# Kernel tuning notes

Measured on AMD Instinct MI355X. Metric: run time of the kernel, lower is better.

## Reference

```python
import jax, jax.numpy as jnp
import numpy as np

BATCH, MAXPV = 32, 50
RULENUM, PROPNUM = 256, 256  # must be equal (eye(rulenum) * property_importance)
ENT_DIM, RULE_DIM = 128, 128
ENTITYNUM = 50000
THRESHOLD = 0.5


def _l2norm(x, eps=1e-12):
    # F.normalize(p=2, dim=-1)
    n = jnp.linalg.norm(x, axis=-1, keepdims=True)
    return x / jnp.clip(n, eps)


def setup_inputs() -> dict:
    key = jax.random.key(0)
    ks = jax.random.split(key, 20)
    d_in = ENT_DIM + RULE_DIM
    inp = {
        'property': jax.random.randint(ks[0], (BATCH, MAXPV), 0, ENTITYNUM),
        'value': jax.random.randint(ks[1], (BATCH, MAXPV), 0, ENTITYNUM),
        'samemask': jax.random.randint(ks[2], (BATCH, MAXPV), 0, 2),
        'padmask': jax.random.randint(ks[3], (BATCH, MAXPV), 0, 2),
        'rule_embedding': jax.random.normal(ks[4], (RULENUM, RULE_DIM), jnp.float32),
        'entity_table': jax.random.normal(ks[5], (ENTITYNUM, ENT_DIM), jnp.float32),
        # Linear weights stored (in, out); concat order in the original is (p_emb, rule_emb)
        'fc1_w': jax.random.normal(ks[6], (d_in, ENT_DIM), jnp.float32),
        'fc1_b': jax.random.normal(ks[7], (ENT_DIM,), jnp.float32) * 0.02,
        'fc2_w': jax.random.normal(ks[8], (d_in, ENT_DIM), jnp.float32),
        'fc2_b': jax.random.normal(ks[9], (ENT_DIM,), jnp.float32) * 0.02,
        'fc3_w': jax.random.normal(ks[10], (d_in, ENT_DIM), jnp.float32),
        'fc3_b': jax.random.normal(ks[11], (ENT_DIM,), jnp.float32) * 0.02,
        'fc4_w': jax.random.normal(ks[12], (ENT_DIM, 1), jnp.float32) * 0.05,
        'fc4_b': jax.random.normal(ks[13], (1,), jnp.float32) * 0.02,
        'fc5_w': jax.random.normal(ks[14], (ENT_DIM, 1), jnp.float32) * 0.05,
        'fc5_b': jax.random.normal(ks[15], (1,), jnp.float32) * 0.02,
        'fc6_w': jax.random.normal(ks[16], (ENT_DIM, ENT_DIM), jnp.float32) * 0.05,
        'fc6_b': jax.random.normal(ks[17], (ENT_DIM,), jnp.float32) * 0.02,
    }
    return inp


def reference(property, value, samemask, padmask, rule_embedding, entity_table,
              fc1_w, fc1_b, fc2_w, fc2_b, fc3_w, fc3_b,
              fc4_w, fc4_b, fc5_w, fc5_b, fc6_w, fc6_b):
    E = entity_table.shape[1]
    R = rule_embedding.shape[0]
    P = R  # propertynum == rulenum (required by eye() regularizer)

    p_emb = _l2norm(entity_table[property])   # (B, M, E)
    v_emb = _l2norm(entity_table[value])      # (B, M, E)
    r_emb = _l2norm(rule_embedding)           # (R, Dr)

    # cat(p, rule) -> Linear decomposed into two smaller matmuls (same math)
    def branch(w, b):
        return p_emb @ w[:E], r_emb @ w[E:] + b  # (B,M,Eo), (R,Eo)

    # s1 branch
    pa, ra = branch(fc1_w, fc1_b)
    h1 = jax.nn.relu(pa[:, None, :, :] + ra[None, :, None, :])   # (B,R,M,E)
    s1 = jax.nn.sigmoid(h1 @ fc4_w + fc4_b)[..., 0]              # (B,R,M)

    # p branch
    pb, rb = branch(fc2_w, fc2_b)
    h2 = jax.nn.relu(pb[:, None, :, :] + rb[None, :, None, :])
    p = jax.nn.sigmoid(h2 @ fc5_w + fc5_b)[..., 0]               # (B,R,M)

    # s2 branch
    pc, rc = branch(fc3_w, fc3_b)
    h3 = jax.nn.relu(pc[:, None, :, :] + rc[None, :, None, :])
    gv = _l2norm(h3 @ fc6_w + fc6_b)                             # (B,R,M,E)
    vb = v_emb[:, None, :, :]                                    # (B,1,M,E)
    denom = jnp.clip(jnp.linalg.norm(vb, axis=-1) * jnp.linalg.norm(gv, axis=-1), 1e-8)
    cos = jnp.sum(vb * gv, axis=-1) / denom
    s2 = 0.5 * cos + 0.5                                         # (B,R,M)

    score = p + (1.0 - p) * s2
    score = jnp.where(samemask[:, None, :] == 1, s1 * score, 1.0 - s1)

    # property importance K: fc1/fc4 on cat(prop_emb, rule_emb)
    prop_emb = _l2norm(entity_table[:P])                         # propertyids = arange(P)
    pi_h = jax.nn.relu((prop_emb @ fc1_w[:E])[None, :, :]
                       + (r_emb @ fc1_w[E:] + fc1_b)[:, None, :])  # (R,P,E)
    pi = jax.nn.sigmoid(pi_h @ fc4_w + fc4_b)[..., 0]            # (R,P)

    rule_mask = jnp.sum(pi * (pi > THRESHOLD), axis=-1) + 1.0    # (R,)

    score = score * padmask[:, None, :].astype(score.dtype)
    score = score * (s1 > THRESHOLD)
    score = jnp.sum(score, axis=-1) / rule_mask[None, :]          # (B,R)
    pooledscore = jnp.max(score, axis=1)                          # (B,)

    diag = jnp.eye(R, dtype=pi.dtype)
    reg = pi * diag + (1.0 - pi) * (1.0 - diag)
    reg = -jnp.log(reg + 1e-8) * (1.0 - diag + diag * R)
    reg_logits = jnp.mean(reg)
    return pooledscore, reg_logits
```

## Files before the change

kernel.cpp:

```cpp
#include <hip/hip_runtime.h>
#include <hip/hip_bf16.h>

#define BATCH 32
#define MAXPV 50
#define RN 256
#define PN 256
#define DIM 128
#define NI (BATCH*MAXPV)

typedef unsigned short u16;
typedef __attribute__((ext_vector_type(8))) short short8;
typedef __attribute__((ext_vector_type(4))) float f32x4;

__device__ float g_pa[NI*DIM], g_pb[NI*DIM], g_pc[NI*DIM];
__device__ float g_pp1[PN*DIM];
__device__ __attribute__((aligned(16))) float g_v[NI*DIM];
__device__ __attribute__((aligned(16))) float g_ra[RN*DIM];
__device__ __attribute__((aligned(16))) float g_rb[RN*DIM];
__device__ float g_rmask[RN], g_regp[RN];
__device__ float g_scores[(size_t)NI*RN];
__device__ short8 g_bfrag[8][4][64];
__device__ __attribute__((aligned(16))) float g_rcA[16*4*64*8];

#define WS_WLS(ws)  ((ws)+4)
#define WS_WLD(ws)  ((ws)+4+1600)

__device__ __forceinline__ float bf2f(u16 u){ return __uint_as_float(((unsigned)u)<<16); }
__device__ __forceinline__ float LD(const void* p, size_t i, bool bf){
    return bf ? bf2f(((const u16*)p)[i]) : ((const float*)p)[i];
}
__device__ __forceinline__ int LDI(const void* p, size_t i, bool w64){
    return w64 ? (int)((const long long*)p)[i] : ((const int*)p)[i];
}
__device__ __forceinline__ short f2bf(float f){
    unsigned u = __float_as_uint(f);
    u = (u + 0x7FFFu + ((u>>16)&1u)) >> 16;
    return (short)u;
}
__device__ __forceinline__ unsigned f2bf2(float x, float y){
    float2 f; f.x=x; f.y=y;
    __hip_bfloat162 h = __float22bfloat162_rn(f);
    union { __hip_bfloat162 h; unsigned u; } c; c.h=h; return c.u;
}
__device__ __forceinline__ bool det_bf16(const void* ent){
    int l = threadIdx.x & 63;
    u16 v = ((const u16*)ent)[(size_t)2*(l*4)*977];
    int e = (v>>7)&0xFF;
    return __popcll(__ballot(e>=120 && e<=133)) >= 48;
}
__device__ __forceinline__ bool det_i64(const void* prop){
    int l = threadIdx.x & 63;
    bool z = (l<32) ? (((const unsigned*)prop)[2*l+1]==0u) : false;
    return __popcll(__ballot(z)) >= 30;
}
__device__ __forceinline__ float wred(float v){
#pragma unroll
    for(int o=32;o;o>>=1) v += __shfl_xor(v,o,64);
    return v;
}
__device__ __forceinline__ double wredd(double v){
#pragma unroll
    for(int o=32;o;o>>=1) v += __shfl_xor(v,o,64);
    return v;
}
__device__ __forceinline__ float wmax(float v){
#pragma unroll
    for(int o=32;o;o>>=1) v = fmaxf(v,__shfl_xor(v,o,64));
    return v;
}

__global__ __launch_bounds__(256) void k_pre(
    const void* __restrict__ ent, const void* __restrict__ rule,
    const void* __restrict__ prop, const void* __restrict__ val,
    const void* __restrict__ same, const void* __restrict__ pad,
    const void* __restrict__ fc6w,
    const void* __restrict__ fc1w, const void* __restrict__ fc2w, const void* __restrict__ fc3w,
    const void* __restrict__ fc1b, const void* __restrict__ fc2b, const void* __restrict__ fc3b,
    int* __restrict__ ws){
    const bool bf = det_bf16(ent);
    const int blk = blockIdx.x, tid = threadIdx.x;
    if(blk >= 379){
        const bool w64 = det_i64(prop);
        const int row = (blk-379)*4 + (tid>>6);
        const int l = tid & 63;
        size_t off = (size_t)LDI(val,row,w64)*DIM;
        float a = LD(ent,off+l,bf), b = LD(ent,off+l+64,bf);
        float n = fmaxf(sqrtf((float)wredd((double)a*a+(double)b*b)), 1e-12f);
        g_v[(size_t)row*DIM+l]=a/n; g_v[(size_t)row*DIM+l+64]=b/n;
        return;
    }
    if(blk >= 372){
        const bool w64 = det_i64(prop);
        int i = (blk-372)*256 + tid;
        if(i < NI){
            int pd = LDI(pad,i,w64);
            if(pd==1){
                int sm = LDI(same,i,w64);
                if(sm==1){
                    int x = atomicAdd(ws+0,1);
                    WS_WLS(ws)[x] = i;
                } else {
                    int x = atomicAdd(ws+1,1);
                    WS_WLD(ws)[x] = i;
                }
            }
        }
        return;
    }
    if(blk >= 364){
        int nt = blk-364;
        int ks = tid>>6, lane = tid&63;
        int n = nt*16 + (lane&15);
        int k0 = ks*32 + (lane>>4)*8;
        short8 v;
#pragma unroll
        for(int j=0;j<8;j++) v[j] = f2bf(LD(fc6w,(size_t)(k0+j)*DIM + n, bf));
        g_bfrag[nt][ks][lane] = v;
        if(nt==0){
            g_rmask[tid] = 1.f; g_regp[tid] = 0.f;
            const bool w64 = det_i64(prop);
            if(tid==0) ws[2] = (bf?1:0) | (w64?2:0);
        }
        return;
    }
    __shared__ float s_w[64*DIM];
    __shared__ __attribute__((aligned(16))) float s_in[16*DIM];
    __shared__ float s_bias[DIM];
    const void* w; size_t woff=0; const void* bptr=nullptr;
    float* out=nullptr; int row0; int mode=0; int srcsel;
    if(blk < 300){
        int wsel = blk/100; row0 = (blk%100)*16; srcsel = 0;
        w   = (wsel==0)?fc1w:(wsel==1)?fc2w:fc3w;
        out = (wsel==0)?g_pa:(wsel==1)?g_pb:g_pc;
    } else if(blk < 348){
        int rblk = blk-300; int wsel = rblk>>4; row0 = (rblk&15)*16; srcsel = 1;
        w    = (wsel==0)?fc1w:(wsel==1)?fc2w:fc3w;
        bptr = (wsel==0)?fc1b:(wsel==1)?fc2b:fc3b;
        woff = DIM*DIM; mode = wsel+1;
    } else { row0=(blk-348)*16; w=fc1w; out=g_pp1; srcsel=2; }
    const bool w64 = (srcsel==0) ? det_i64(prop) : false;
    {
        const int l = tid & 63;
        for(int it=0; it<4; it++){
            int lr = it*4 + (tid>>6);
            int row = row0 + lr;
            const void* src; size_t off;
            if(srcsel==0){ src=ent;  off=(size_t)LDI(prop,row,w64)*DIM; }
            else if(srcsel==1){ src=rule; off=(size_t)row*DIM; }
            else { src=ent; off=(size_t)row*DIM; }
            float a = LD(src,off+l,bf), b = LD(src,off+l+64,bf);
            float n = fmaxf(sqrtf((float)wredd((double)a*a+(double)b*b)), 1e-12f);
            s_in[lr*DIM+l]=a/n; s_in[lr*DIM+l+64]=b/n;
        }
    }
    if(tid<DIM) s_bias[tid] = bptr ? LD(bptr,tid,bf) : 0.f;
    const int j = tid & 127;
    const int rb8 = (tid>>7)*8;
    double acc[8] = {0,0,0,0,0,0,0,0};
    for(int half=0; half<2; half++){
        __syncthreads();
        for(int t=tid; t<64*DIM; t+=256)
            s_w[t] = LD(w, woff + (size_t)(half*64 + (t>>7))*DIM + (t&127), bf);
        __syncthreads();
        for(int k=0;k<64;k+=4){
            const float w0 = s_w[(k+0)*DIM + j];
            const float w1 = s_w[(k+1)*DIM + j];
            const float w2 = s_w[(k+2)*DIM + j];
            const float w3 = s_w[(k+3)*DIM + j];
#pragma unroll
            for(int rr=0;rr<8;rr++){
                const float4 in4 = *(const float4*)&s_in[(rb8+rr)*DIM + half*64 + k];
                acc[rr] += (double)in4.x*(double)w0;
                acc[rr] += (double)in4.y*(double)w1;
                acc[rr] += (double)in4.z*(double)w2;
                acc[rr] += (double)in4.w*(double)w3;
            }
        }
    }
    const double bj = (double)s_bias[j];
#pragma unroll
    for(int rr=0;rr<8;rr++){
        const int row = row0 + rb8 + rr;
        const float vv = (float)(bj + acc[rr]);
        if(mode==0)      out[(size_t)row*DIM + j] = vv;
        else if(mode==1) g_ra[(size_t)row*DIM + j] = vv;
        else if(mode==2) g_rb[(size_t)row*DIM + j] = vv;
        else {
            int mt=row>>4, am=row&15, ks=j>>5, quad=(j>>3)&3, jj=j&7;
            g_rcA[((mt*4+ks)*64 + quad*16+am)*8 + jj] = vv;
        }
    }
}

__global__ __launch_bounds__(256) void k_score(
    const void* __restrict__ fc4w, const void* __restrict__ fc4b,
    const void* __restrict__ fc5w, const void* __restrict__ fc5b,
    const void* __restrict__ fc6b, const int* __restrict__ ws){
    const int blk = blockIdx.x, tid = threadIdx.x;
    const int fl = ws[2];
    const bool bf = fl & 1;
    if(blk < 64){
        __shared__ float s_a[4][DIM];
        __shared__ double s_pf4[DIM];
        const int i0 = blk*4;
        if(tid<DIM) s_pf4[tid]=(double)LD(fc4w,tid,bf);
        for(int t=tid; t<4*DIM; t+=256){
            int ii=t>>7, k=t&127;
            s_a[ii][k] = g_pp1[(size_t)(i0+ii)*DIM+k];
        }
        __syncthreads();
        const int r = tid;
        const float4* rap = (const float4*)&g_ra[(size_t)r*DIM];
        double d0=0.0, d1=0.0, d2=0.0, d3=0.0;
#pragma unroll 4
        for(int x=0; x<32; x++){
            const float4 ra = rap[x];
#pragma unroll
            for(int cc=0; cc<4; cc++){
                const int k = x*4 + cc;
                const float rav = (cc==0)?ra.x:(cc==1)?ra.y:(cc==2)?ra.z:ra.w;
                const double f4k = s_pf4[k];
                d0 += (double)fmaxf(s_a[0][k]+rav,0.f)*f4k;
                d1 += (double)fmaxf(s_a[1][k]+rav,0.f)*f4k;
                d2 += (double)fmaxf(s_a[2][k]+rav,0.f)*f4k;
                d3 += (double)fmaxf(s_a[3][k]+rav,0.f)*f4k;
            }
        }
        const double b4 = (double)LD(fc4b,0,bf);
        double d[4] = {d0,d1,d2,d3};
        float mask_sum = 0.f, reg_sum = 0.f;
#pragma unroll
        for(int ii=0;ii<4;ii++){
            int p = i0 + ii;
            double sd = d[ii] + b4;
            float piv = 1.f/(1.f+expf(-(float)sd));
            if(sd > 0.0) mask_sum += piv;
            float eff = (p==r) ? piv : (1.f - piv);
            float wgt = (p==r) ? (float)RN : 1.f;
            reg_sum += -logf(eff + 1e-8f)*wgt;
        }
        atomicAdd(&g_rmask[r], mask_sum);
        atomicAdd(&g_regp[r], reg_sum);
        return;
    }
    int w2 = blk - 64;
    const int ns4 = ws[0]*4;

    __shared__ float s_pa[DIM], s_pb[DIM], s_pc[DIM], s_v[DIM], s_f4[DIM], s_f5[DIM];
    __shared__ double s_gd[2][64];
    __shared__ float s_gq[2][64];
    __shared__ double s_pd[2][128];
    __shared__ float s_s1[64], s_p[64];
    __shared__ float s_st[64][4][2];

    if(w2 >= ns4){
        int t2 = w2 - ns4;
        if(t2 >= 2*ws[1]) return;
        const int i = WS_WLD(ws)[t2>>1];
        const int sub = t2 & 1;
        if(tid < 128){
            s_pa[tid] = g_pa[(size_t)i*DIM + tid];
            s_f4[tid] = LD(fc4w,tid,bf);
        }
        __syncthreads();
        const int rr = tid & 127, half = tid >> 7;
        const int r = sub*128 + rr;
        const float4* rap = (const float4*)&g_ra[(size_t)r*DIM + half*64];
        double d = 0.0;
#pragma unroll 4
        for(int x=0; x<16; x++){
            const float4 ra = rap[x];
            const int k = half*64 + x*4;
            d += (double)fmaxf(s_pa[k+0]+ra.x,0.f)*(double)s_f4[k+0];
            d += (double)fmaxf(s_pa[k+1]+ra.y,0.f)*(double)s_f4[k+1];
            d += (double)fmaxf(s_pa[k+2]+ra.z,0.f)*(double)s_f4[k+2];
            d += (double)fmaxf(s_pa[k+3]+ra.w,0.f)*(double)s_f4[k+3];
        }
        s_pd[half][rr] = d;
        __syncthreads();
        if(tid < 128){
            const double b4 = (double)LD(fc4b,0,bf);
            double sd = (s_pd[0][tid] + s_pd[1][tid]) + b4;
            float s1v = 1.f/(1.f+expf(-(float)sd));
            g_scores[(size_t)i*RN + sub*128 + tid] = (sd > 0.0) ? (1.f - s1v) : 0.f;
        }
        return;
    }

    const int i = WS_WLS(ws)[w2>>2];
    const int q4 = w2 & 3;

    if(tid < DIM){
        s_pa[tid] = g_pa[(size_t)i*DIM + tid];
        s_pb[tid] = g_pb[(size_t)i*DIM + tid];
        s_pc[tid] = g_pc[(size_t)i*DIM + tid];
        s_f4[tid] = LD(fc4w,tid,bf);
        s_f5[tid] = LD(fc5w,tid,bf);
    } else if(tid < 192){
        const int ll = tid - 128;
        s_v[ll]    = g_v[(size_t)i*DIM + ll];
        s_v[ll+64] = g_v[(size_t)i*DIM + ll + 64];
    }
    __syncthreads();

    const int rr = tid & 63, wv = tid >> 6;
    const int r = q4*64 + rr;
    if(wv < 2){
        const float4* rap = (const float4*)&g_ra[(size_t)r*DIM + wv*64];
        double d = 0.0;
#pragma unroll 4
        for(int x=0; x<16; x++){
            const float4 ra = rap[x];
            const int k = wv*64 + x*4;
            d += (double)fmaxf(s_pa[k+0]+ra.x,0.f)*(double)s_f4[k+0];
            d += (double)fmaxf(s_pa[k+1]+ra.y,0.f)*(double)s_f4[k+1];
            d += (double)fmaxf(s_pa[k+2]+ra.z,0.f)*(double)s_f4[k+2];
            d += (double)fmaxf(s_pa[k+3]+ra.w,0.f)*(double)s_f4[k+3];
        }
        s_gd[wv][rr] = d;
    } else {
        const int hh = wv - 2;
        const float4* rbp = (const float4*)&g_rb[(size_t)r*DIM + hh*64];
        float pq = 0.f;
#pragma unroll 4
        for(int x=0; x<16; x++){
            const float4 rb = rbp[x];
            const int k = hh*64 + x*4;
            pq = fmaf(fmaxf(s_pb[k+0]+rb.x,0.f), s_f5[k+0], pq);
            pq = fmaf(fmaxf(s_pb[k+1]+rb.y,0.f), s_f5[k+1], pq);
            pq = fmaf(fmaxf(s_pb[k+2]+rb.z,0.f), s_f5[k+2], pq);
            pq = fmaf(fmaxf(s_pb[k+3]+rb.w,0.f), s_f5[k+3], pq);
        }
        s_gq[hh][rr] = pq;
    }
    __syncthreads();
    if(tid < 64){
        const double b4 = (double)LD(fc4b,0,bf);
        double sd = (s_gd[0][tid] + s_gd[1][tid]) + b4;
        float s1v = 1.f/(1.f+expf(-(float)sd));
        s_s1[tid] = (sd > 0.0) ? s1v : -s1v;
    } else if(tid < 128){
        const float b5 = LD(fc5b,0,bf);
        float pq = s_gq[0][tid-64] + s_gq[1][tid-64];
        s_p[tid-64] = 1.f/(1.f+expf(-(pq + b5)));
    }
    __syncthreads();

    const int w = tid>>6, l = tid&63;
    const int am = l&15, quad = l>>4;
    short8 bA[4], bB[4];
#pragma unroll
    for(int ks=0; ks<4; ks++){ bA[ks]=g_bfrag[2*w][ks][l]; bB[ks]=g_bfrag[2*w+1][ks][l]; }
    const int n0 = w*32 + am, n1 = n0 + 16;
    const float v0 = s_v[n0], v1 = s_v[n1];
    const float b60 = LD(fc6b, n0, bf), b61 = LD(fc6b, n1, bf);
    float vl = s_v[l], vh = s_v[l+64];
    const float nvb = sqrtf(wred(vl*vl + vh*vh));

    for(int mtl=0; mtl<4; mtl++){
        const int mt = q4*4 + mtl;
        float4 c[8];
#pragma unroll
        for(int ks=0; ks<4; ks++){
            const float* rp = &g_rcA[((mt*4+ks)*64 + l)*8];
            c[2*ks]   = *(const float4*)rp;
            c[2*ks+1] = *(const float4*)(rp+4);
        }
        short8 a[4];
#pragma unroll
        for(int ks=0; ks<4; ks++){
            const float4 p0 = *(const float4*)&s_pc[ks*32 + quad*8];
            const float4 p1 = *(const float4*)&s_pc[ks*32 + quad*8 + 4];
            const float4 c0 = c[2*ks], c1 = c[2*ks+1];
            union { short8 s; unsigned u[4]; } t;
            t.u[0] = f2bf2(fmaxf(p0.x+c0.x,0.f), fmaxf(p0.y+c0.y,0.f));
            t.u[1] = f2bf2(fmaxf(p0.z+c0.z,0.f), fmaxf(p0.w+c0.w,0.f));
            t.u[2] = f2bf2(fmaxf(p1.x+c1.x,0.f), fmaxf(p1.y+c1.y,0.f));
            t.u[3] = f2bf2(fmaxf(p1.z+c1.z,0.f), fmaxf(p1.w+c1.w,0.f));
            a[ks] = t.s;
        }
        f32x4 acc0 = {0.f,0.f,0.f,0.f}, acc1 = {0.f,0.f,0.f,0.f};
#pragma unroll
        for(int ks=0; ks<4; ks++){
            acc0 = __builtin_amdgcn_mfma_f32_16x16x32_bf16(a[ks], bA[ks], acc0, 0,0,0);
            acc1 = __builtin_amdgcn_mfma_f32_16x16x32_bf16(a[ks], bB[ks], acc1, 0,0,0);
        }
#pragma unroll
        for(int q=0; q<4; q++){
            float x0 = acc0[q] + b60;
            float x1 = acc1[q] + b61;
            float ss = x0*x0 + x1*x1;
            float dv = x0*v0 + x1*v1;
#pragma unroll
            for(int o=1;o<16;o<<=1){ ss += __shfl_xor(ss,o,64); dv += __shfl_xor(dv,o,64); }
            if(am==0){
                int row = mtl*16 + quad*4 + q;
                s_st[row][w][0] = ss;
                s_st[row][w][1] = dv;
            }
        }
    }
    __syncthreads();
    if(tid < 64){
        const int r2 = q4*64 + tid;
        float ss = s_st[tid][0][0]+s_st[tid][1][0]+s_st[tid][2][0]+s_st[tid][3][0];
        float dv = s_st[tid][0][1]+s_st[tid][1][1]+s_st[tid][2][1]+s_st[tid][3][1];
        float s1 = fabsf(s_s1[tid]);
        float gate = (s_s1[tid] > 0.f) ? 1.f : 0.f;
        float pp = s_p[tid];
        float nx = sqrtf(ss);
        float clipnx = fmaxf(nx, 1e-12f);
        float gvn = nx/clipnx;
        float denom = fmaxf(nvb*gvn, 1e-8f);
        float cosv = (dv/clipnx)/denom;
        float s2 = 0.5f*cosv + 0.5f;
        float sc = s1*(pp + (1.f-pp)*s2);
        g_scores[(size_t)i*RN + r2] = sc * gate;
    }
}

__global__ void k_fin(float* __restrict__ out, const void* __restrict__ pad,
                      const int* __restrict__ ws){
    const bool w64 = (ws[2] & 2) != 0;
    const int blk = blockIdx.x, tid = threadIdx.x;
    const int w = tid>>6, l = tid&63;
    __shared__ float s[4];
    if(blk < 32){
        __shared__ float s_padf[MAXPV];
        if(tid < MAXPV) s_padf[tid] = LDI(pad, (size_t)blk*MAXPV + tid, w64) ? 1.f : 0.f;
        __syncthreads();
        float ssum = 0.f;
#pragma unroll 10
        for(int pv=0; pv<MAXPV; pv++){
            float v = g_scores[((size_t)blk*MAXPV + pv)*RN + tid];
            ssum += (s_padf[pv] != 0.f) ? v : 0.f;
        }
        float sc = ssum / g_rmask[tid];
        float m = wmax(sc);
        if(l==0) s[w]=m;
        __syncthreads();
        if(tid==0) out[blk] = fmaxf(fmaxf(s[0],s[1]), fmaxf(s[2],s[3]));
    } else {
        float v = g_regp[tid];
        v = wred(v);
        if(l==0) s[w]=v;
        __syncthreads();
        if(tid==0) out[32] = (s[0]+s[1]+s[2]+s[3]) / (float)(RN*PN);
    }
}

extern "C" void kernel_launch(void* const* d_in, const int* in_sizes, int n_in,
                              void* d_out, int out_size, void* d_ws, size_t ws_size,
                              hipStream_t stream){
    int map[18]; for(int i=0;i<18;i++) map[i]=i;
    if(n_in>=18 && in_sizes[0]==6400000){
        const int a[18] = {14,17,16,13,15,0,2,1,4,3,6,5,8,7,10,9,12,11};
        for(int i=0;i<18;i++) map[i]=a[i];
    }
    const void* prop = d_in[map[0]];
    const void* val  = d_in[map[1]];
    const void* same = d_in[map[2]];
    const void* pad  = d_in[map[3]];
    const void* rule = d_in[map[4]];
    const void* ent  = d_in[map[5]];
    const void* fc1w = d_in[map[6]];
    const void* fc1b = d_in[map[7]];
    const void* fc2w = d_in[map[8]];
    const void* fc2b = d_in[map[9]];
    const void* fc3w = d_in[map[10]];
    const void* fc3b = d_in[map[11]];
    const void* fc4w = d_in[map[12]];
    const void* fc4b = d_in[map[13]];
    const void* fc5w = d_in[map[14]];
    const void* fc5b = d_in[map[15]];
    const void* fc6w = d_in[map[16]];
    const void* fc6b = d_in[map[17]];

    hipMemsetAsync(d_ws, 0, 16, stream);
    k_pre<<<779, 256, 0, stream>>>(ent, rule, prop, val, same, pad, fc6w,
                                   fc1w, fc2w, fc3w, fc1b, fc2b, fc3b, (int*)d_ws);
    k_score<<<64 + 6400, 256, 0, stream>>>(fc4w, fc4b, fc5w, fc5b, fc6b,
                                           (const int*)d_ws);
    k_fin<<<33, 256, 0, stream>>>((float*)d_out, pad, (const int*)d_ws);
}
```

Measured before the change: 176.3 us.

## Fuse three kernels into one persistent cooperative kernel with grid syncs

Replaces the memset plus three kernel launches with a single cooperative kernel of 512 blocks. The blocks loop over the old per-block work items and use grid-wide syncs between the pre, score and final phases. The score phase only iterates over the work count actually produced, rather than launching 6400 blocks that mostly exit early. The goal is to remove launch gaps and empty-block overhead, at the cost of grid-sync latency and fewer resident blocks for the heavy phases. If the cooperative launch fails, it falls back to the old three-kernel path.

```diff
diff --git a/kernel.cpp b/kernel.cpp
--- a/kernel.cpp
+++ b/kernel.cpp
@@ -1,5 +1,8 @@
 #include <hip/hip_runtime.h>
 #include <hip/hip_bf16.h>
+#include <hip/hip_cooperative_groups.h>
+
+namespace cg = cooperative_groups;
 
 #define BATCH 32
 #define MAXPV 50
@@ -25,6 +28,26 @@
 #define WS_WLS(ws)  ((ws)+4)
 #define WS_WLD(ws)  ((ws)+4+1600)
 
+#define P1_W(sm)    ((float*)(sm))
+#define P1_IN(sm)   ((float*)((sm)+32768))
+#define P1_B(sm)    ((float*)((sm)+40960))
+#define SM1_BYTES   41472
+#define P2_PA(sm)   ((float*)(sm))
+#define P2_PB(sm)   ((float*)((sm)+512))
+#define P2_PC(sm)   ((float*)((sm)+1024))
+#define P2_V(sm)    ((float*)((sm)+1536))
+#define P2_F4(sm)   ((float*)((sm)+2048))
+#define P2_F5(sm)   ((float*)((sm)+2560))
+#define P2_GD(sm)   ((double*)((sm)+3072))
+#define P2_GQ(sm)   ((float*)((sm)+4096))
+#define P2_PD(sm)   ((double*)((sm)+4608))
+#define P2_S1(sm)   ((float*)((sm)+6656))
+#define P2_P(sm)    ((float*)((sm)+6912))
+#define P2_ST(sm)   ((float*)((sm)+7168))
+#define P2_PADF(sm) ((float*)((sm)+9216))
+#define P2_S(sm)    ((float*)((sm)+9424))
+#define SM2_BYTES   9440
+
 __device__ __forceinline__ float bf2f(u16 u){ return __uint_as_float(((unsigned)u)<<16); }
 __device__ __forceinline__ float LD(const void* p, size_t i, bool bf){
     return bf ? bf2f(((const u16*)p)[i]) : ((const float*)p)[i];
@@ -69,16 +92,13 @@
     return v;
 }
 
-__global__ __launch_bounds__(256) void k_pre(
-    const void* __restrict__ ent, const void* __restrict__ rule,
-    const void* __restrict__ prop, const void* __restrict__ val,
-    const void* __restrict__ same, const void* __restrict__ pad,
-    const void* __restrict__ fc6w,
-    const void* __restrict__ fc1w, const void* __restrict__ fc2w, const void* __restrict__ fc3w,
-    const void* __restrict__ fc1b, const void* __restrict__ fc2b, const void* __restrict__ fc3b,
-    int* __restrict__ ws){
+__device__ __forceinline__ void do_pre_item(int blk, char* sm,
+    const void* ent, const void* rule, const void* prop, const void* val,
+    const void* same, const void* pad, const void* fc6w,
+    const void* fc1w, const void* fc2w, const void* fc3w,
+    const void* fc1b, const void* fc2b, const void* fc3b, int* ws){
     const bool bf = det_bf16(ent);
-    const int blk = blockIdx.x, tid = threadIdx.x;
+    const int tid = threadIdx.x;
     if(blk >= 379){
         const bool w64 = det_i64(prop);
         const int row = (blk-379)*4 + (tid>>6);
@@ -95,8 +115,8 @@
         if(i < NI){
             int pd = LDI(pad,i,w64);
             if(pd==1){
-                int sm = LDI(same,i,w64);
-                if(sm==1){
+                int smk = LDI(same,i,w64);
+                if(smk==1){
                     int x = atomicAdd(ws+0,1);
                     WS_WLS(ws)[x] = i;
                 } else {
@@ -123,9 +143,9 @@
         }
         return;
     }
-    __shared__ float s_w[64*DIM];
-    __shared__ __attribute__((aligned(16))) float s_in[16*DIM];
-    __shared__ float s_bias[DIM];
+    float* s_w  = P1_W(sm);
+    float* s_in = P1_IN(sm);
+    float* s_bias = P1_B(sm);
     const void* w; size_t woff=0; const void* bptr=nullptr;
     float* out=nullptr; int row0; int mode=0; int srcsel;
     if(blk < 300){
@@ -192,22 +212,19 @@
     }
 }
 
-__global__ __launch_bounds__(256) void k_score(
-    const void* __restrict__ fc4w, const void* __restrict__ fc4b,
-    const void* __restrict__ fc5w, const void* __restrict__ fc5b,
-    const void* __restrict__ fc6b, const int* __restrict__ ws){
-    const int blk = blockIdx.x, tid = threadIdx.x;
-    const int fl = ws[2];
+__device__ __forceinline__ void do_score_item(int blk, char* sm,
+    const void* fc4w, const void* fc4b, const void* fc5w, const void* fc5b,
+    const void* fc6b, const int* ws){
+    const int tid = threadIdx.x;
+    volatile const int* wsv = ws;
+    const int fl = wsv[2];
     const bool bf = fl & 1;
     if(blk < 64){
-        __shared__ float s_a[4][DIM];
-        __shared__ double s_pf4[DIM];
+        float* s_a = P2_PA(sm);
+        double* s_pf4 = P2_GD(sm);
         const int i0 = blk*4;
         if(tid<DIM) s_pf4[tid]=(double)LD(fc4w,tid,bf);
-        for(int t=tid; t<4*DIM; t+=256){
-            int ii=t>>7, k=t&127;
-            s_a[ii][k] = g_pp1[(size_t)(i0+ii)*DIM+k];
-        }
+        for(int t=tid; t<4*DIM; t+=256) s_a[t] = g_pp1[(size_t)i0*DIM + t];
         __syncthreads();
         const int r = tid;
         const float4* rap = (const float4*)&g_ra[(size_t)r*DIM];
@@ -220,10 +237,10 @@
                 const int k = x*4 + cc;
                 const float rav = (cc==0)?ra.x:(cc==1)?ra.y:(cc==2)?ra.z:ra.w;
                 const double f4k = s_pf4[k];
-                d0 += (double)fmaxf(s_a[0][k]+rav,0.f)*f4k;
-                d1 += (double)fmaxf(s_a[1][k]+rav,0.f)*f4k;
-                d2 += (double)fmaxf(s_a[2][k]+rav,0.f)*f4k;
-                d3 += (double)fmaxf(s_a[3][k]+rav,0.f)*f4k;
+                d0 += (double)fmaxf(s_a[0*DIM+k]+rav,0.f)*f4k;
+                d1 += (double)fmaxf(s_a[1*DIM+k]+rav,0.f)*f4k;
+                d2 += (double)fmaxf(s_a[2*DIM+k]+rav,0.f)*f4k;
+                d3 += (double)fmaxf(s_a[3*DIM+k]+rav,0.f)*f4k;
             }
         }
         const double b4 = (double)LD(fc4b,0,bf);
@@ -244,18 +261,16 @@
         return;
     }
     int w2 = blk - 64;
-    const int ns4 = ws[0]*4;
-
-    __shared__ float s_pa[DIM], s_pb[DIM], s_pc[DIM], s_v[DIM], s_f4[DIM], s_f5[DIM];
-    __shared__ double s_gd[2][64];
-    __shared__ float s_gq[2][64];
-    __shared__ double s_pd[2][128];
-    __shared__ float s_s1[64], s_p[64];
-    __shared__ float s_st[64][4][2];
+    const int ns4 = wsv[0]*4;
+
+    float* s_pa = P2_PA(sm); float* s_pb = P2_PB(sm); float* s_pc = P2_PC(sm);
+    float* s_v  = P2_V(sm);  float* s_f4 = P2_F4(sm); float* s_f5 = P2_F5(sm);
+    double* s_gd = P2_GD(sm); float* s_gq = P2_GQ(sm); double* s_pd = P2_PD(sm);
+    float* s_s1 = P2_S1(sm); float* s_p = P2_P(sm); float* s_st = P2_ST(sm);
 
     if(w2 >= ns4){
         int t2 = w2 - ns4;
-        if(t2 >= 2*ws[1]) return;
+        if(t2 >= 2*wsv[1]) return;
         const int i = WS_WLD(ws)[t2>>1];
         const int sub = t2 & 1;
         if(tid < 128){
@@ -276,11 +291,11 @@
             d += (double)fmaxf(s_pa[k+2]+ra.z,0.f)*(double)s_f4[k+2];
             d += (double)fmaxf(s_pa[k+3]+ra.w,0.f)*(double)s_f4[k+3];
         }
-        s_pd[half][rr] = d;
+        s_pd[half*128+rr] = d;
         __syncthreads();
         if(tid < 128){
             const double b4 = (double)LD(fc4b,0,bf);
-            double sd = (s_pd[0][tid] + s_pd[1][tid]) + b4;
+            double sd = (s_pd[tid] + s_pd[128+tid]) + b4;
             float s1v = 1.f/(1.f+expf(-(float)sd));
             g_scores[(size_t)i*RN + sub*128 + tid] = (sd > 0.0) ? (1.f - s1v) : 0.f;
         }
@@ -317,7 +332,7 @@
             d += (double)fmaxf(s_pa[k+2]+ra.z,0.f)*(double)s_f4[k+2];
             d += (double)fmaxf(s_pa[k+3]+ra.w,0.f)*(double)s_f4[k+3];
         }
-        s_gd[wv][rr] = d;
+        s_gd[wv*64+rr] = d;
     } else {
         const int hh = wv - 2;
         const float4* rbp = (const float4*)&g_rb[(size_t)r*DIM + hh*64];
@@ -331,17 +346,17 @@
             pq = fmaf(fmaxf(s_pb[k+2]+rb.z,0.f), s_f5[k+2], pq);
             pq = fmaf(fmaxf(s_pb[k+3]+rb.w,0.f), s_f5[k+3], pq);
         }
-        s_gq[hh][rr] = pq;
+        s_gq[hh*64+rr] = pq;
     }
     __syncthreads();
     if(tid < 64){
         const double b4 = (double)LD(fc4b,0,bf);
-        double sd = (s_gd[0][tid] + s_gd[1][tid]) + b4;
+        double sd = (s_gd[tid] + s_gd[64+tid]) + b4;
         float s1v = 1.f/(1.f+expf(-(float)sd));
         s_s1[tid] = (sd > 0.0) ? s1v : -s1v;
     } else if(tid < 128){
         const float b5 = LD(fc5b,0,bf);
-        float pq = s_gq[0][tid-64] + s_gq[1][tid-64];
+        float pq = s_gq[tid-64] + s_gq[64+tid-64];
         s_p[tid-64] = 1.f/(1.f+expf(-(pq + b5)));
     }
     __syncthreads();
@@ -395,16 +410,16 @@
             for(int o=1;o<16;o<<=1){ ss += __shfl_xor(ss,o,64); dv += __shfl_xor(dv,o,64); }
             if(am==0){
                 int row = mtl*16 + quad*4 + q;
-                s_st[row][w][0] = ss;
-                s_st[row][w][1] = dv;
+                s_st[(row*4+w)*2+0] = ss;
+                s_st[(row*4+w)*2+1] = dv;
             }
         }
     }
     __syncthreads();
     if(tid < 64){
         const int r2 = q4*64 + tid;
-        float ss = s_st[tid][0][0]+s_st[tid][1][0]+s_st[tid][2][0]+s_st[tid][3][0];
-        float dv = s_st[tid][0][1]+s_st[tid][1][1]+s_st[tid][2][1]+s_st[tid][3][1];
+        float ss = s_st[(tid*4+0)*2]+s_st[(tid*4+1)*2]+s_st[(tid*4+2)*2]+s_st[(tid*4+3)*2];
+        float dv = s_st[(tid*4+0)*2+1]+s_st[(tid*4+1)*2+1]+s_st[(tid*4+2)*2+1]+s_st[(tid*4+3)*2+1];
         float s1 = fabsf(s_s1[tid]);
         float gate = (s_s1[tid] > 0.f) ? 1.f : 0.f;
         float pp = s_p[tid];
@@ -419,14 +434,14 @@
     }
 }
 
-__global__ void k_fin(float* __restrict__ out, const void* __restrict__ pad,
-                      const int* __restrict__ ws){
-    const bool w64 = (ws[2] & 2) != 0;
-    const int blk = blockIdx.x, tid = threadIdx.x;
+__device__ __forceinline__ void do_fin_item(int blk, char* sm,
+    float* out, const void* pad, const int* ws){
+    const bool w64 = (((volatile const int*)ws)[2] & 2) != 0;
+    const int tid = threadIdx.x;
     const int w = tid>>6, l = tid&63;
-    __shared__ float s[4];
+    float* s = P2_S(sm);
     if(blk < 32){
-        __shared__ float s_padf[MAXPV];
+        float* s_padf = P2_PADF(sm);
         if(tid < MAXPV) s_padf[tid] = LDI(pad, (size_t)blk*MAXPV + tid, w64) ? 1.f : 0.f;
         __syncthreads();
         float ssum = 0.f;
@@ -447,6 +462,55 @@
         __syncthreads();
         if(tid==0) out[32] = (s[0]+s[1]+s[2]+s[3]) / (float)(RN*PN);
     }
+}
+
+__global__ __launch_bounds__(256) void k_all(
+    const void* ent, const void* rule, const void* prop, const void* val,
+    const void* same, const void* pad, const void* fc6w,
+    const void* fc1w, const void* fc2w, const void* fc3w,
+    const void* fc1b, const void* fc2b, const void* fc3b,
+    const void* fc4w, const void* fc4b, const void* fc5w, const void* fc5b,
+    const void* fc6b, float* out, int* ws){
+    cg::grid_group gg = cg::this_grid();
+    __shared__ __attribute__((aligned(16))) char sm[SM1_BYTES];
+    if(blockIdx.x==0 && threadIdx.x<4) ws[threadIdx.x]=0;
+    gg.sync();
+    for(int it=blockIdx.x; it<779; it+=(int)gridDim.x){
+        __syncthreads();
+        do_pre_item(it, sm, ent,rule,prop,val,same,pad,fc6w,
+                    fc1w,fc2w,fc3w,fc1b,fc2b,fc3b,ws);
+    }
+    gg.sync();
+    const int total2 = 64 + 4*((volatile int*)ws)[0] + 2*((volatile int*)ws)[1];
+    for(int it=blockIdx.x; it<total2; it+=(int)gridDim.x){
+        __syncthreads();
+        do_score_item(it, sm, fc4w,fc4b,fc5w,fc5b,fc6b,ws);
+    }
+    gg.sync();
+    if(blockIdx.x < 33){
+        __syncthreads();
+        do_fin_item(blockIdx.x, sm, out, pad, ws);
+    }
+}
+
+__global__ __launch_bounds__(256) void k_pre(
+    const void* ent, const void* rule, const void* prop, const void* val,
+    const void* same, const void* pad, const void* fc6w,
+    const void* fc1w, const void* fc2w, const void* fc3w,
+    const void* fc1b, const void* fc2b, const void* fc3b, int* ws){
+    __shared__ __attribute__((aligned(16))) char sm[SM1_BYTES];
+    do_pre_item(blockIdx.x, sm, ent,rule,prop,val,same,pad,fc6w,
+                fc1w,fc2w,fc3w,fc1b,fc2b,fc3b,ws);
+}
+__global__ __launch_bounds__(256) void k_score(
+    const void* fc4w, const void* fc4b, const void* fc5w, const void* fc5b,
+    const void* fc6b, const int* ws){
+    __shared__ __attribute__((aligned(16))) char sm[SM2_BYTES];
+    do_score_item(blockIdx.x, sm, fc4w,fc4b,fc5w,fc5b,fc6b,ws);
+}
+__global__ void k_fin(float* out, const void* pad, const int* ws){
+    __shared__ __attribute__((aligned(16))) char sm[SM2_BYTES];
+    do_fin_item(blockIdx.x, sm, out, pad, ws);
 }
 
 extern "C" void kernel_launch(void* const* d_in, const int* in_sizes, int n_in,
@@ -475,11 +539,20 @@
     const void* fc5b = d_in[map[15]];
     const void* fc6w = d_in[map[16]];
     const void* fc6b = d_in[map[17]];
-
-    hipMemsetAsync(d_ws, 0, 16, stream);
-    k_pre<<<779, 256, 0, stream>>>(ent, rule, prop, val, same, pad, fc6w,
-                                   fc1w, fc2w, fc3w, fc1b, fc2b, fc3b, (int*)d_ws);
-    k_score<<<64 + 6400, 256, 0, stream>>>(fc4w, fc4b, fc5w, fc5b, fc6b,
-                                           (const int*)d_ws);
-    k_fin<<<33, 256, 0, stream>>>((float*)d_out, pad, (const int*)d_ws);
-}
+    float* outp = (float*)d_out;
+    int* wsp = (int*)d_ws;
+
+    void* ka[20] = {&ent,&rule,&prop,&val,&same,&pad,&fc6w,
+                    &fc1w,&fc2w,&fc3w,&fc1b,&fc2b,&fc3b,
+                    &fc4w,&fc4b,&fc5w,&fc5b,&fc6b,&outp,&wsp};
+    hipError_t e = hipLaunchCooperativeKernel((const void*)k_all, dim3(512), dim3(256),
+                                              ka, 0, stream);
+    if(e != hipSuccess){
+        hipMemsetAsync(d_ws, 0, 16, stream);
+        k_pre<<<779, 256, 0, stream>>>(ent, rule, prop, val, same, pad, fc6w,
+                                       fc1w, fc2w, fc3w, fc1b, fc2b, fc3b, wsp);
+        k_score<<<64 + 6400, 256, 0, stream>>>(fc4w, fc4b, fc5w, fc5b, fc6b,
+                                               (const int*)wsp);
+        k_fin<<<33, 256, 0, stream>>>(outp, pad, (const int*)wsp);
+    }
+}
```

Result: slower. 383.4 us (+117.5%).
